# Kernel tuning notes

Hardware: AMD Instinct MI355X
Metric: run time of the kernel (lower is better)

Reference implementation:

```python
import jax, jax.numpy as jnp
import numpy as np

B, L, V = 4, 1024, 1280
N_EMBD, N_BIN, N_HID = 768, 8, 32
HORIZON = 10.0


def setup_inputs() -> dict:
    key = jax.random.key(0)
    k_h, k_age, k_gap, k_tgt, k_w1, k_w2 = jax.random.split(key, 6)
    h = jax.random.normal(k_h, (B, L, N_EMBD), dtype=jnp.float32)
    # ages increase along a trajectory; gaps in [0, 2) years
    age = jnp.sort(jax.random.uniform(k_age, (B, L), dtype=jnp.float32) * 80.0, axis=-1)
    targets_age = age + jax.random.uniform(k_gap, (B, L), dtype=jnp.float32) * 2.0
    delta_t = targets_age - age  # passed to forward but unused (as in torch source)
    targets = jax.random.randint(k_tgt, (B, L), 0, V, dtype=jnp.int32)
    W1 = jax.random.normal(k_w1, (N_EMBD, N_BIN * N_HID), dtype=jnp.float32) * 0.02
    W2 = jax.random.normal(k_w2, (N_HID, V), dtype=jnp.float32) * 0.02
    return {"h": h, "age": age, "targets_age": targets_age, "delta_t": delta_t,
            "targets": targets, "W1": W1, "W2": W2}


def _time_to_event(age, targets_age, targets):
    # delta_full[b,i,j] = targets_age[b,j] - age[b,i]
    delta_full = targets_age[:, None, :] - age[:, :, None]  # (B,L,L)
    i_idx = jnp.arange(L)
    # torch.triu(diagonal=0): keep targets[b,j] where j>=i, else 0
    upper = (i_idx[None, :] >= i_idx[:, None])  # (L,L) mask, col>=row
    targets_exp = jnp.where(upper[None, :, :], targets[:, None, :], 0)  # (B,L,L)
    # scatter-reduce amin of position index j into vocab slot targets_exp[b,i,j]
    # sentinel L plays the role of torch's -1 (min over srcs ignores it; src<=L-1)
    b_ix = jnp.arange(B)[:, None, None]
    r_ix = i_idx[None, :, None]
    src = jnp.broadcast_to(i_idx[None, None, :], (B, L, L)).astype(jnp.int32)
    token_index = jnp.full((B, L, V), L, dtype=jnp.int32)
    token_index = token_index.at[b_ix, r_ix, targets_exp].min(src)
    no_event = token_index == L
    token_index = jnp.where(no_event, L - 1, token_index)  # (B,L,V)
    tte = jnp.take_along_axis(delta_full, token_index, axis=-1)  # (B,L,V)
    return tte, no_event, token_index


def reference(h, age, targets_age, delta_t, targets, W1, W2):
    # two dense projections: (B,L,E) -> (B,L,n_bin,n_hid) -> (B,L,n_bin,V)
    x = jnp.einsum('ble,eo->blo', h, W1).reshape(B, L, N_BIN, N_HID)
    logits = jnp.einsum('blnh,hv->blnv', x, W2)
    tte, no_event, _ = _time_to_event(age, targets_age, targets)
    edges = jnp.linspace(0.0, HORIZON, N_BIN + 1)
    lo = edges[:-1][None, None, :, None]
    hi = edges[1:][None, None, :, None]
    t = tte[:, :, None, :]  # (B,L,1,V)
    censor_mask = ((t >= lo) & (t < hi)) | no_event[:, :, None, :]  # (B,L,n_bin,V)
    return logits, tte, censor_mask
```

## Files before the change

### kernel.cpp

```cpp
#include <hip/hip_runtime.h>
#include <hip/hip_bf16.h>

#define B_   4
#define L_   1024
#define V_   1280
#define NE_  768
#define NB_  8
#define NH_  32
#define NO_  (NB_*NH_)
#define BL_  (B_*L_)
#define M2_  (BL_*NB_)

typedef __attribute__((ext_vector_type(8))) short bf16x8;
typedef __attribute__((ext_vector_type(4))) float floatx4;

__device__ __forceinline__ unsigned short f2bf(float f) {
    unsigned int u = __float_as_uint(f);
    u += 0x7FFFu + ((u >> 16) & 1u);
    return (unsigned short)(u >> 16);
}

#define H4_N   (BL_*NE_/4)
#define W1T_N  (NO_*NE_)
#define W2T_N  (V_*NH_)
#define K0_TOT (H4_N + W1T_N + W2T_N)

__global__ __launch_bounds__(256) void k0_pack(const float* __restrict__ h,
                                               const float* __restrict__ W1,
                                               const float* __restrict__ W2,
                                               unsigned short* __restrict__ hb,
                                               unsigned short* __restrict__ W1T,
                                               unsigned short* __restrict__ W2T) {
    int id = blockIdx.x * 256 + threadIdx.x;
    if (id < H4_N) {
        float4 v = ((const float4*)h)[id];
        ushort4 o;
        o.x = f2bf(v.x); o.y = f2bf(v.y); o.z = f2bf(v.z); o.w = f2bf(v.w);
        ((ushort4*)hb)[id] = o;
    } else if (id < H4_N + W1T_N) {
        int j = id - H4_N;
        int o = j / NE_;
        int k = j - o * NE_;
        W1T[j] = f2bf(W1[(size_t)k * NO_ + o]);
    } else if (id < K0_TOT) {
        int j = id - H4_N - W1T_N;
        int v = j >> 5;
        int k = j & 31;
        W2T[j] = f2bf(W2[(size_t)k * V_ + v]);
    }
}

__global__ __launch_bounds__(256) void k1_gemm(const unsigned short* __restrict__ hb,
                                               const unsigned short* __restrict__ W1T,
                                               unsigned short* __restrict__ Xb) {
    __shared__ short A_lds[64][40];
    __shared__ short Bt_lds[64][40];

    const int t      = threadIdx.x;
    const int m0     = blockIdx.x * 64;
    const int n0     = blockIdx.y * 64;
    const int l      = t & 63;
    const int w      = t >> 6;
    const int lane15 = l & 15;
    const int quad   = l >> 4;

    const int srow = t >> 2;
    const int sq   = (t & 3) * 8;

    const unsigned short* aptr = hb  + (size_t)(m0 + srow) * NE_ + sq;
    const unsigned short* bptr = W1T + (size_t)(n0 + srow) * NE_ + sq;

    floatx4 acc[4];
#pragma unroll
    for (int i = 0; i < 4; ++i) acc[i] = (floatx4){0.f, 0.f, 0.f, 0.f};

    bf16x8 av = *(const bf16x8*)aptr;
    bf16x8 bv = *(const bf16x8*)bptr;

    for (int k0 = 0; k0 < NE_; k0 += 32) {
        __syncthreads();
        *(bf16x8*)&A_lds[srow][sq]  = av;
        *(bf16x8*)&Bt_lds[srow][sq] = bv;
        __syncthreads();
        if (k0 + 32 < NE_) {
            av = *(const bf16x8*)(aptr + k0 + 32);
            bv = *(const bf16x8*)(bptr + k0 + 32);
        }
        bf16x8 af = *(bf16x8*)&A_lds[w * 16 + lane15][quad * 8];
#pragma unroll
        for (int nt = 0; nt < 4; ++nt) {
            bf16x8 bf = *(bf16x8*)&Bt_lds[nt * 16 + lane15][quad * 8];
            acc[nt] = __builtin_amdgcn_mfma_f32_16x16x32_bf16(af, bf, acc[nt], 0, 0, 0);
        }
    }

    const int rbase = m0 + w * 16 + quad * 4;
#pragma unroll
    for (int nt = 0; nt < 4; ++nt)
#pragma unroll
        for (int r = 0; r < 4; ++r)
            Xb[(size_t)(rbase + r) * NO_ + n0 + nt * 16 + lane15] = f2bf(acc[nt][r]);
}

__global__ __launch_bounds__(256) void k2_logits(const unsigned short* __restrict__ Xb,
                                                 const unsigned short* __restrict__ W2T,
                                                 float* __restrict__ outL) {
    const int t      = threadIdx.x;
    const int m0     = blockIdx.x * 64;
    const int l      = t & 63;
    const int w      = t >> 6;
    const int lane15 = l & 15;
    const int quad   = l >> 4;

    const int m = m0 + w * 16 + lane15;
    const bf16x8 af = *(const bf16x8*)(Xb + (size_t)m * NH_ + quad * 8);

    const int rbase = m0 + w * 16 + quad * 4;

#pragma unroll 4
    for (int nt = 0; nt < V_ / 16; ++nt) {
        bf16x8 bf = *(const bf16x8*)(W2T + (size_t)(nt * 16 + lane15) * NH_ + quad * 8);
        floatx4 c = (floatx4){0.f, 0.f, 0.f, 0.f};
        c = __builtin_amdgcn_mfma_f32_16x16x32_bf16(af, bf, c, 0, 0, 0);
#pragma unroll
        for (int r = 0; r < 4; ++r)
            outL[(size_t)(rbase + r) * V_ + nt * 16 + lane15] = c[r];
    }
}

#define K3_S 32

__global__ __launch_bounds__(256) void k3_tte(const float* __restrict__ age,
                                              const float* __restrict__ tage,
                                              const int*   __restrict__ targets,
                                              float* __restrict__ outT,
                                              float* __restrict__ outM) {
    __shared__ int   tg[L_];
    __shared__ float ta[L_];
    __shared__ float ag[K3_S];

    const int t      = threadIdx.x;
    const int v      = blockIdx.x * 256 + t;
    const int istart = blockIdx.y * K3_S;
    const int iend   = istart + K3_S;
    const int b      = blockIdx.z;

    for (int j = t; j < L_; j += 256) {
        tg[j] = targets[(size_t)b * L_ + j];
        ta[j] = tage[(size_t)b * L_ + j];
    }
    if (t < K3_S) ag[t] = age[(size_t)b * L_ + istart + t];
    __syncthreads();

    int cur = L_;
    for (int i = L_ - 1; i >= istart; --i) {
        const int ti = tg[i];
        if (ti == v) cur = i;
        if (i < iend) {
            int idx = cur;
            if (v == 0 && i >= 1) idx = 0;
            const bool noev = (idx == L_);
            const int  ic   = noev ? (L_ - 1) : idx;
            const float tte = ta[ic] - ag[i - istart];

            outT[((size_t)(b * L_ + i)) * V_ + v] = tte;

            const size_t mb = ((size_t)(b * L_ + i)) * NB_ * V_ + v;
#pragma unroll
            for (int n = 0; n < NB_; ++n) {
                const float lo = n * 1.25f;
                const float hi = (n + 1) * 1.25f;
                const bool in_bin = (tte >= lo) && (tte < hi);
                outM[mb + (size_t)n * V_] = (in_bin || noev) ? 1.0f : 0.0f;
            }
        }
    }
}

extern "C" void kernel_launch(void* const* d_in, const int* in_sizes, int n_in,
                              void* d_out, int out_size, void* d_ws, size_t ws_size,
                              hipStream_t stream) {
    const float* h       = (const float*)d_in[0];
    const float* age     = (const float*)d_in[1];
    const float* tage    = (const float*)d_in[2];
    const int*   targets = (const int*)  d_in[4];
    const float* W1      = (const float*)d_in[5];
    const float* W2      = (const float*)d_in[6];

    float* out  = (float*)d_out;
    float* outL = out;
    float* outT = out + (size_t)BL_ * NB_ * V_;
    float* outM = outT + (size_t)BL_ * V_;

    char* ws = (char*)d_ws;
    unsigned short* hb  = (unsigned short*)(ws);
    unsigned short* W1T = (unsigned short*)(ws + 6291456);
    unsigned short* W2T = (unsigned short*)(ws + 6291456 + 393216);
    unsigned short* Xb  = (unsigned short*)(ws + 6291456 + 393216 + 81920);

    k0_pack  <<<(K0_TOT + 255) / 256, 256, 0, stream>>>(h, W1, W2, hb, W1T, W2T);
    k1_gemm  <<<dim3(BL_/64, NO_/64), 256, 0, stream>>>(hb, W1T, Xb);
    k2_logits<<<M2_/64, 256, 0, stream>>>(Xb, W2T, outL);
    k3_tte   <<<dim3(V_/256, L_/K3_S, B_), 256, 0, stream>>>(age, tage, targets, outT, outM);
}
```

Measured before the change: 425.2 us.

## Precompute chunk suffix occurrences for TTE and vectorize logits stores

The time-to-event kernel used to make each block rescan targets from the end of the sequence down to its chunk, which costs quadratic work over the chunks. A new scan kernel records the next occurrence of each vocab token at every 32-position chunk boundary, so each TTE block scans only its own 32 rows. The logits kernel also swaps the MFMA operand roles so each lane holds four consecutive vocab outputs and writes them as one float4 store instead of four scattered scalar stores. The cost is an extra kernel launch and a workspace buffer for the suffix table.

Result: no change. 420.0 us (-1.2%).

```diff
diff --git a/kernel.cpp b/kernel.cpp
--- a/kernel.cpp
+++ b/kernel.cpp
@@ -113,66 +113,86 @@
     const int quad   = l >> 4;
 
     const int m = m0 + w * 16 + lane15;
-    const bf16x8 af = *(const bf16x8*)(Xb + (size_t)m * NH_ + quad * 8);
-
-    const int rbase = m0 + w * 16 + quad * 4;
+    const bf16x8 bfrag = *(const bf16x8*)(Xb + (size_t)m * NH_ + quad * 8);
+
+    float* orow = outL + (size_t)m * V_ + quad * 4;
+    const unsigned short* wrow = W2T + (size_t)lane15 * NH_ + quad * 8;
 
 #pragma unroll 4
     for (int nt = 0; nt < V_ / 16; ++nt) {
-        bf16x8 bf = *(const bf16x8*)(W2T + (size_t)(nt * 16 + lane15) * NH_ + quad * 8);
+        const bf16x8 afrag = *(const bf16x8*)(wrow + (size_t)nt * 16 * NH_);
         floatx4 c = (floatx4){0.f, 0.f, 0.f, 0.f};
-        c = __builtin_amdgcn_mfma_f32_16x16x32_bf16(af, bf, c, 0, 0, 0);
-#pragma unroll
-        for (int r = 0; r < 4; ++r)
-            outL[(size_t)(rbase + r) * V_ + nt * 16 + lane15] = c[r];
+        c = __builtin_amdgcn_mfma_f32_16x16x32_bf16(afrag, bfrag, c, 0, 0, 0);
+        *(floatx4*)(orow + nt * 16) = c;
     }
 }
 
 #define K3_S 32
-
-__global__ __launch_bounds__(256) void k3_tte(const float* __restrict__ age,
-                                              const float* __restrict__ tage,
-                                              const int*   __restrict__ targets,
-                                              float* __restrict__ outT,
-                                              float* __restrict__ outM) {
-    __shared__ int   tg[L_];
+#define NCH  (L_/K3_S)
+
+__global__ __launch_bounds__(256) void k3a_scan(const int* __restrict__ targets,
+                                                int* __restrict__ sufocc) {
+    __shared__ int tg[L_];
+    const int t = threadIdx.x;
+    const int v = blockIdx.x * 256 + t;
+    const int b = blockIdx.z;
+
+    for (int j = t; j < L_; j += 256) tg[j] = targets[(size_t)b * L_ + j];
+    __syncthreads();
+
+    int cur = L_;
+    for (int i = L_ - 1; i >= 0; --i) {
+        if (tg[i] == v) cur = i;
+        if ((i & (K3_S - 1)) == 0)
+            sufocc[(size_t)(b * NCH + (i >> 5)) * V_ + v] = cur;
+    }
+}
+
+__global__ __launch_bounds__(256) void k3b_tte(const float* __restrict__ age,
+                                               const float* __restrict__ tage,
+                                               const int*   __restrict__ targets,
+                                               const int*   __restrict__ sufocc,
+                                               float* __restrict__ outT,
+                                               float* __restrict__ outM) {
     __shared__ float ta[L_];
+    __shared__ int   tg[K3_S];
     __shared__ float ag[K3_S];
 
     const int t      = threadIdx.x;
     const int v      = blockIdx.x * 256 + t;
-    const int istart = blockIdx.y * K3_S;
-    const int iend   = istart + K3_S;
+    const int y      = blockIdx.y;
+    const int istart = y * K3_S;
     const int b      = blockIdx.z;
 
-    for (int j = t; j < L_; j += 256) {
-        tg[j] = targets[(size_t)b * L_ + j];
-        ta[j] = tage[(size_t)b * L_ + j];
-    }
-    if (t < K3_S) ag[t] = age[(size_t)b * L_ + istart + t];
+    for (int j = t; j < L_; j += 256) ta[j] = tage[(size_t)b * L_ + j];
+    if (t < K3_S) {
+        tg[t] = targets[(size_t)b * L_ + istart + t];
+        ag[t] = age[(size_t)b * L_ + istart + t];
+    }
     __syncthreads();
 
-    int cur = L_;
-    for (int i = L_ - 1; i >= istart; --i) {
-        const int ti = tg[i];
-        if (ti == v) cur = i;
-        if (i < iend) {
-            int idx = cur;
-            if (v == 0 && i >= 1) idx = 0;
-            const bool noev = (idx == L_);
-            const int  ic   = noev ? (L_ - 1) : idx;
-            const float tte = ta[ic] - ag[i - istart];
-
-            outT[((size_t)(b * L_ + i)) * V_ + v] = tte;
-
-            const size_t mb = ((size_t)(b * L_ + i)) * NB_ * V_ + v;
-#pragma unroll
-            for (int n = 0; n < NB_; ++n) {
-                const float lo = n * 1.25f;
-                const float hi = (n + 1) * 1.25f;
-                const bool in_bin = (tte >= lo) && (tte < hi);
-                outM[mb + (size_t)n * V_] = (in_bin || noev) ? 1.0f : 0.0f;
-            }
+    int cur = (y == NCH - 1) ? L_
+                             : sufocc[(size_t)(b * NCH + y + 1) * V_ + v];
+
+    for (int i = K3_S - 1; i >= 0; --i) {
+        const int gi = istart + i;
+        if (tg[i] == v) cur = gi;
+
+        int idx = cur;
+        if (v == 0 && gi >= 1) idx = 0;
+        const bool noev = (idx == L_);
+        const int  ic   = noev ? (L_ - 1) : idx;
+        const float tte = ta[ic] - ag[i];
+
+        outT[((size_t)(b * L_ + gi)) * V_ + v] = tte;
+
+        const size_t mb = ((size_t)(b * L_ + gi)) * NB_ * V_ + v;
+#pragma unroll
+        for (int n = 0; n < NB_; ++n) {
+            const float lo = n * 1.25f;
+            const float hi = (n + 1) * 1.25f;
+            const bool in_bin = (tte >= lo) && (tte < hi);
+            outM[mb + (size_t)n * V_] = (in_bin || noev) ? 1.0f : 0.0f;
         }
     }
 }
@@ -197,9 +217,11 @@
     unsigned short* W1T = (unsigned short*)(ws + 6291456);
     unsigned short* W2T = (unsigned short*)(ws + 6291456 + 393216);
     unsigned short* Xb  = (unsigned short*)(ws + 6291456 + 393216 + 81920);
+    int*            suf = (int*)           (ws + 6291456 + 393216 + 81920 + 2097152);
 
     k0_pack  <<<(K0_TOT + 255) / 256, 256, 0, stream>>>(h, W1, W2, hb, W1T, W2T);
     k1_gemm  <<<dim3(BL_/64, NO_/64), 256, 0, stream>>>(hb, W1T, Xb);
     k2_logits<<<M2_/64, 256, 0, stream>>>(Xb, W2T, outL);
-    k3_tte   <<<dim3(V_/256, L_/K3_S, B_), 256, 0, stream>>>(age, tage, targets, outT, outM);
-}
+    k3a_scan <<<dim3(V_/256, 1, B_), 256, 0, stream>>>(targets, suf);
+    k3b_tte  <<<dim3(V_/256, L_/K3_S, B_), 256, 0, stream>>>(age, tage, targets, suf, outT, outM);
+}
```
